# Performance work log

Hardware: AMD Instinct MI355X
Metric: run time of the kernel (lower is better)

Reference implementation:

```python
import jax, jax.numpy as jnp
import numpy as np

HID, NH, HD, KTS = 512, 8, 64, 4
BATCH, SEQ = 2, 1024
CLIP, AMIN, AMAX = 2.0, 1e-4, 0.9995
ROPE_BASE = 10000.0


def _rmsnorm(x, w, eps=1e-5):
    rms = jnp.sqrt(jnp.mean(x * x, axis=-1, keepdims=True) + eps)
    return x / rms * w


def _rope(q, k, base=ROPE_BASE):
    # q,k: [B,T,H,D], D even -> rotate-half formulation (split halves, not interleaved)
    T, D = q.shape[1], q.shape[-1]
    half = D // 2
    pos = jnp.arange(T, dtype=q.dtype)
    inv_freq = 1.0 / (base ** (jnp.arange(half, dtype=q.dtype) / half))
    ang = pos[:, None] * inv_freq[None, :]            # [T, half]
    cos = jnp.cos(ang)[None, :, None, :]
    sin = jnp.sin(ang)[None, :, None, :]
    def rot(x):
        x1, x2 = x[..., :half], x[..., half:]
        return jnp.concatenate([x1 * cos - x2 * sin, x1 * sin + x2 * cos], axis=-1)
    return rot(q), rot(k)


def setup_inputs() -> dict:
    key = jax.random.key(0)
    ks = jax.random.split(key, 10)
    def xavier(k, shape):
        lim = float(np.sqrt(6.0 / (shape[0] + shape[1])))
        return jax.random.uniform(k, shape, jnp.float32, -lim, lim)
    x = jax.random.normal(ks[0], (BATCH, SEQ, HID), jnp.float32)
    mask = jnp.ones((BATCH, SEQ), jnp.int32)
    qW = xavier(ks[1], (HID, HID))
    kW = xavier(ks[2], (HID, HID))
    vW = xavier(ks[3], (HID, HID))
    oW = xavier(ks[4], (HID, HID))
    ob = jnp.zeros((HID,), jnp.float32)
    # alpha bias from geometric half-lives [32,128,512,2048]
    half_lives = np.array([32.0 * (4.0 ** i) for i in range(KTS)], dtype=np.float64)
    alphas = np.clip(np.exp(-np.log(2.0) / half_lives), AMIN, AMAX)
    alphas = np.tile(alphas, NH)
    ab = jnp.asarray(np.log(alphas / (1.0 - alphas)), jnp.float32)
    aW = 0.01 * jax.random.normal(ks[5], (NH * KTS, HID), jnp.float32)
    mW = 0.01 * jax.random.normal(ks[6], (NH * KTS, HID), jnp.float32)
    mb = jnp.zeros((NH * KTS,), jnp.float32)
    in_w = jnp.ones((HID,), jnp.float32)
    kn_w = jnp.ones((HD,), jnp.float32)
    vn_w = jnp.ones((HD,), jnp.float32)
    ln_w = jnp.ones((HID,), jnp.float32)
    ln_b = jnp.zeros((HID,), jnp.float32)
    return dict(x=x, in_w=in_w, qW=qW, kW=kW, vW=vW, aW=aW, ab=ab, mW=mW, mb=mb,
                oW=oW, ob=ob, kn_w=kn_w, vn_w=vn_w, ln_w=ln_w, ln_b=ln_b, mask=mask)


def reference(x, in_w, qW, kW, vW, aW, ab, mW, mb, oW, ob, kn_w, vn_w, ln_w, ln_b, mask):
    B, T, _ = x.shape
    xn = _rmsnorm(x, in_w)
    q = (xn @ qW.T).reshape(B, T, NH, HD)
    k = (xn @ kW.T).reshape(B, T, NH, HD)
    v = (xn @ vW.T).reshape(B, T, NH, HD)
    q, k = _rope(q, k)
    k = _rmsnorm(k, kn_w)
    v = _rmsnorm(v, vn_w)
    alpha = jnp.clip(jax.nn.sigmoid(xn @ aW.T + ab), AMIN, AMAX).reshape(B, T, NH, KTS)
    mix = jax.nn.softmax((xn @ mW.T + mb).reshape(B, T, NH, KTS), axis=-1)
    m = mask.astype(jnp.float32)
    c = float(np.sqrt(HD)) * CLIP

    def step(h, inp):
        # h: [B,H,K,D,D] fp32 state; delta-rule write + multi-timescale decay + norm clip
        q_t, k_t, v_t, a_t, mx_t, m_t = inp
        outer = (k_t * m_t[:, None, None])[:, :, None, :, None] * v_t[:, :, None, None, :]
        h = h * a_t[..., None, None] + outer
        norm = jnp.sqrt(jnp.sum(h * h, axis=(-2, -1), keepdims=True))
        h = h * jnp.minimum(c / (norm + 1e-6), 1.0)
        y = jnp.einsum('bhd,bhkde->bhke', q_t, h)
        return h, jnp.einsum('bhk,bhkd->bhd', mx_t, y)

    h0 = jnp.zeros((B, NH, KTS, HD, HD), jnp.float32)
    tm = lambda a: jnp.moveaxis(a, 1, 0)  # time-major
    xs = (tm(q), tm(k), tm(v), tm(alpha), tm(mix), m.T)
    _, ys = jax.lax.scan(jax.checkpoint(step), h0, xs)  # ys: [T,B,H,D]
    y = jnp.moveaxis(ys, 0, 1).reshape(B, T, HID)
    out = y @ oW.T + ob  # dropout p=0 (eval)
    r = x + out
    mu = jnp.mean(r, axis=-1, keepdims=True)
    var = jnp.mean((r - mu) ** 2, axis=-1, keepdims=True)
    return (r - mu) / jnp.sqrt(var + 1e-5) * ln_w + ln_b
```

## Files before the change

### kernel.cpp

```cpp
#include <hip/hip_runtime.h>
#include <math.h>

#define SEQT 1024
#define NTOK 2048
#define HIDN 512
#define NHD 8
#define HDIM 64
#define KTSN 4

__device__ __forceinline__ float wred(float v) {
#pragma unroll
  for (int off = 32; off; off >>= 1) v += __shfl_xor(v, off, 64);
  return v;
}

template <int CTRL>
__device__ __forceinline__ float rra(float v) {
  return v + __int_as_float(__builtin_amdgcn_update_dpp(
                 0, __float_as_int(v), CTRL, 0xf, 0xf, true));
}
__device__ __forceinline__ float rlane(float v, int l) {
  return __int_as_float(__builtin_amdgcn_readlane(__float_as_int(v), l));
}
__device__ __forceinline__ float wsum64_fast(float v) {
  v = rra<0x121>(v);
  v = rra<0x122>(v);
  v = rra<0x124>(v);
  v = rra<0x128>(v);
  return (rlane(v, 0) + rlane(v, 16)) + (rlane(v, 32) + rlane(v, 48));
}

__global__ __launch_bounds__(256) void k_rmsnorm_in(
    const float* __restrict__ x, const float* __restrict__ w, float* __restrict__ xn) {
  int m = blockIdx.x;
  int tid = threadIdx.x;
  const float* row = x + (size_t)m * HIDN;
  float2 v = *(const float2*)(row + tid * 2);
  float ss = wred(v.x * v.x + v.y * v.y);
  __shared__ float red[4];
  int lane = tid & 63, wv = tid >> 6;
  if (lane == 0) red[wv] = ss;
  __syncthreads();
  float tot = red[0] + red[1] + red[2] + red[3];
  float inv = rsqrtf(tot * (1.0f / HIDN) + 1e-5f);
  float2 wv2 = *(const float2*)(w + tid * 2);
  float2 o;
  o.x = v.x * inv * wv2.x;
  o.y = v.y * inv * wv2.y;
  *(float2*)(xn + (size_t)m * HIDN + tid * 2) = o;
}

__global__ __launch_bounds__(256) void k_gemm_nt(
    const float* __restrict__ A, const float* __restrict__ B, float* __restrict__ C, int N) {
  __shared__ __align__(16) float As[32][68];
  __shared__ __align__(16) float Bs[32][68];
  int tid = threadIdx.x;
  int m0 = blockIdx.x * 64, n0 = blockIdx.y * 64;
  int tm = tid >> 4, tn = tid & 15;
  float acc[4][4] = {};
  int rr = tid >> 2, cc = (tid & 3) * 8;
  for (int k0 = 0; k0 < HIDN; k0 += 32) {
    const float* s0 = A + (size_t)(m0 + rr) * HIDN + k0 + cc;
    float4 a0 = *(const float4*)s0;
    float4 a1 = *(const float4*)(s0 + 4);
    As[cc + 0][rr] = a0.x; As[cc + 1][rr] = a0.y; As[cc + 2][rr] = a0.z; As[cc + 3][rr] = a0.w;
    As[cc + 4][rr] = a1.x; As[cc + 5][rr] = a1.y; As[cc + 6][rr] = a1.z; As[cc + 7][rr] = a1.w;
    int bn = n0 + rr;
    float4 b0 = make_float4(0.f, 0.f, 0.f, 0.f), b1 = make_float4(0.f, 0.f, 0.f, 0.f);
    if (bn < N) {
      const float* s1 = B + (size_t)bn * HIDN + k0 + cc;
      b0 = *(const float4*)s1;
      b1 = *(const float4*)(s1 + 4);
    }
    Bs[cc + 0][rr] = b0.x; Bs[cc + 1][rr] = b0.y; Bs[cc + 2][rr] = b0.z; Bs[cc + 3][rr] = b0.w;
    Bs[cc + 4][rr] = b1.x; Bs[cc + 5][rr] = b1.y; Bs[cc + 6][rr] = b1.z; Bs[cc + 7][rr] = b1.w;
    __syncthreads();
#pragma unroll
    for (int kk = 0; kk < 32; ++kk) {
      float4 a4 = *(const float4*)&As[kk][tm * 4];
      float4 b4 = *(const float4*)&Bs[kk][tn * 4];
      float aa[4] = {a4.x, a4.y, a4.z, a4.w};
      float bb[4] = {b4.x, b4.y, b4.z, b4.w};
#pragma unroll
      for (int i = 0; i < 4; ++i)
#pragma unroll
        for (int j = 0; j < 4; ++j) acc[i][j] += aa[i] * bb[j];
    }
    __syncthreads();
  }
#pragma unroll
  for (int i = 0; i < 4; ++i) {
    int mr = m0 + tm * 4 + i;
#pragma unroll
    for (int j = 0; j < 4; ++j) {
      int nc = n0 + tn * 4 + j;
      if (nc < N) C[(size_t)mr * N + nc] = acc[i][j];
    }
  }
}

__global__ __launch_bounds__(256) void k_rope_table(float2* __restrict__ tab) {
  int idx = blockIdx.x * 256 + threadIdx.x;
  int t = idx >> 5, j = idx & 31;
  float invf = (float)exp2(-(double)j * (13.287712379549449 / 32.0));
  float ang = (float)t * invf;
  double s, c;
  sincos((double)ang, &s, &c);
  tab[idx] = make_float2((float)c, (float)s);
}

__global__ __launch_bounds__(256) void k_postproc(
    const float* __restrict__ q_in, const float* __restrict__ k_in, const float* __restrict__ v_in,
    const float* __restrict__ a_pre, const float* __restrict__ m_pre,
    const float* __restrict__ ab, const float* __restrict__ mb,
    const float* __restrict__ kn_w, const float* __restrict__ vn_w,
    const float2* __restrict__ tab,
    float* __restrict__ qh, float* __restrict__ kh, float* __restrict__ vh,
    float* __restrict__ av, float* __restrict__ mv) {
  int wid = blockIdx.x * 4 + (threadIdx.x >> 6);
  int lane = threadIdx.x & 63;
  int b = wid >> 13;
  int rem = wid & 8191;
  int t = rem >> 3;
  int h = rem & 7;
  size_t src = (size_t)(b * SEQT + t) * HIDN + h * HDIM + lane;
  float qv = q_in[src], kv = k_in[src], vv = v_in[src];
  float2 cs = tab[t * 32 + (lane & 31)];
  float qpart = __shfl_xor(qv, 32, 64);
  float kpart = __shfl_xor(kv, 32, 64);
  float qr = (lane < 32) ? (qv * cs.x - qpart * cs.y) : (qpart * cs.y + qv * cs.x);
  float kr = (lane < 32) ? (kv * cs.x - kpart * cs.y) : (kpart * cs.y + kv * cs.x);
  float kss = wred(kr * kr);
  float kn = kr * rsqrtf(kss * (1.0f / HDIM) + 1e-5f) * kn_w[lane];
  float vss = wred(vv * vv);
  float vn = vv * rsqrtf(vss * (1.0f / HDIM) + 1e-5f) * vn_w[lane];
  size_t dst = ((size_t)(b * NHD + h) * SEQT + t) * HDIM + lane;
  qh[dst] = qr;
  kh[dst] = kn;
  vh[dst] = vn;
  if (lane < 4) {
    int col = h * 4 + lane;
    float pa = a_pre[(size_t)(b * SEQT + t) * 32 + col] + ab[col];
    float al = 1.0f / (1.0f + expf(-pa));
    al = fminf(fmaxf(al, 1e-4f), 0.9995f);
    float pm = m_pre[(size_t)(b * SEQT + t) * 32 + col] + mb[col];
    float mx = pm;
    mx = fmaxf(mx, __shfl_xor(mx, 1, 64));
    mx = fmaxf(mx, __shfl_xor(mx, 2, 64));
    float e = expf(pm - mx);
    float sum = e;
    sum += __shfl_xor(sum, 1, 64);
    sum += __shfl_xor(sum, 2, 64);
    size_t adst = ((size_t)(b * NHD + h) * KTSN + lane) * SEQT + t;
    av[adst] = al;
    mv[adst] = e / sum;
  }
}

#define G16(X) \
  X(0, 0) X(1, 1) X(2, 2) X(3, 3) X(4, 0) X(5, 1) X(6, 2) X(7, 3) \
  X(8, 0) X(9, 1) X(10, 2) X(11, 3) X(12, 0) X(13, 1) X(14, 2) X(15, 3)

#define DECLH(g, a) float h##g = 0.f;

#define UPDH(g, a)                                \
  {                                               \
    float ks = rlane(kqC, g);                     \
    h##g = fmaf(h##g, ag, ks * vem);              \
    sq##a = fmaf(h##g, h##g, sq##a);              \
  }

#define YUPH(g, a)                                \
  {                                               \
    float qs = rlane(kqC, 16 + (g));              \
    y##a = fmaf(qs, h##g, y##a);                  \
  }

__global__ __launch_bounds__(256, 1) void k_scan(
    const float* __restrict__ qh, const float* __restrict__ kh, const float* __restrict__ vh,
    const float* __restrict__ av, const float* __restrict__ mv, const int* __restrict__ mask,
    float* __restrict__ y0p, float* __restrict__ y1p, float* __restrict__ y2p,
    float* __restrict__ y3p) {
  int c = blockIdx.x;
  int kt = c & 3;
  int bh = c >> 2;
  int b = bh >> 3;
  int h = bh & 7;
  int tid = threadIdx.x;
  int w = tid >> 6;
  int lane = tid & 63;
  int dbase = w * 16;

  const float* kp = kh + (size_t)bh * SEQT * HDIM;
  const float* qp = qh + (size_t)bh * SEQT * HDIM;
  const float* vp = vh + (size_t)bh * SEQT * HDIM;
  const float* ap = av + (size_t)c * SEQT;
  const float* mp = mv + (size_t)c * SEQT;
  const int* mk = mask + (size_t)b * SEQT;
  float* ysel = (kt == 0) ? y0p : (kt == 1) ? y1p : (kt == 2) ? y2p : y3p;
  float* ypo = ysel + (size_t)(b * SEQT) * HIDN + h * HDIM + lane;

  __shared__ __align__(16) float sqb[2][4];
  __shared__ __align__(16) float ypart[2][4][64];

  G16(DECLH)
  float gprev = 1.0f;

  int off = lane & 15;
  const float* kqbase = ((lane >> 4) & 1) ? qp : kp;
  int kqidx = dbase + off;

  float kqC = kqbase[kqidx];
  float kqD = kqbase[(size_t)1 * HDIM + kqidx];
  float kqE = kqbase[(size_t)2 * HDIM + kqidx];
  float vC = vp[lane];
  float vD = vp[(size_t)1 * HDIM + lane];
  float vE = vp[(size_t)2 * HDIM + lane];
  float aC = ap[0], aD = ap[1], aE = ap[2];
  float mxC = mp[0], mxD = mp[1], mxE = mp[2];
  float mC = (float)mk[0], mD = (float)mk[1], mE = (float)mk[2];

  for (int t = 0; t < SEQT; ++t) {
    int t3 = t + 3;
    if (t3 > SEQT - 1) t3 = SEQT - 1;
    float kqN = kqbase[(size_t)t3 * HDIM + kqidx];
    float vN = vp[(size_t)t3 * HDIM + lane];
    float aN = ap[t3];
    float mxN = mp[t3];
    float mN = (float)mk[t3];

    float ag = aC * gprev;
    float vem = vC * mC;
    float sq0 = 0.f, sq1 = 0.f, sq2 = 0.f, sq3 = 0.f;
    G16(UPDH)
    float y0 = 0.f, y1 = 0.f, y2 = 0.f, y3 = 0.f;
    G16(YUPH)
    float sqw = wsum64_fast((sq0 + sq1) + (sq2 + sq3));
    float yp = (y0 + y1) + (y2 + y3);

    int P = t & 1;
    if (lane == 0) sqb[P][w] = sqw;
    ypart[P][w][lane] = yp;
    __syncthreads();
    float4 sq4 = *(const float4*)&sqb[P][0];
    float sqt = (sq4.x + sq4.y) + (sq4.z + sq4.w);
    float g = fminf(16.0f * rsqrtf(sqt), 1.0f);
    if (w == 0) {
      float ys = (ypart[P][0][lane] + ypart[P][1][lane]) +
                 (ypart[P][2][lane] + ypart[P][3][lane]);
      ypo[(size_t)t * HIDN] = (mxC * g) * ys;
    }
    gprev = g;

    kqC = kqD; kqD = kqE; kqE = kqN;
    vC = vD; vD = vE; vE = vN;
    aC = aD; aD = aE; aE = aN;
    mxC = mxD; mxD = mxE; mxE = mxN;
    mC = mD; mD = mE; mE = mN;
  }
}

__global__ __launch_bounds__(256) void k_gemm_out(
    const float* __restrict__ y0, const float* __restrict__ y1,
    const float* __restrict__ y2, const float* __restrict__ y3,
    const float* __restrict__ oW, const float* __restrict__ ob,
    const float* __restrict__ x, float* __restrict__ r) {
  __shared__ __align__(16) float As[32][68];
  __shared__ __align__(16) float Bs[32][68];
  int tid = threadIdx.x;
  int m0 = blockIdx.x * 64, n0 = blockIdx.y * 64;
  int tm = tid >> 4, tn = tid & 15;
  float acc[4][4] = {};
  int rr = tid >> 2, cc = (tid & 3) * 8;
  for (int k0 = 0; k0 < HIDN; k0 += 32) {
    size_t aoff = (size_t)(m0 + rr) * HIDN + k0 + cc;
#pragma unroll
    for (int half = 0; half < 2; ++half) {
      size_t sh = aoff + half * 4;
      float4 p0 = *(const float4*)(y0 + sh);
      float4 p1 = *(const float4*)(y1 + sh);
      float4 p2 = *(const float4*)(y2 + sh);
      float4 p3 = *(const float4*)(y3 + sh);
      int cbase = cc + half * 4;
      As[cbase + 0][rr] = p0.x + p1.x + p2.x + p3.x;
      As[cbase + 1][rr] = p0.y + p1.y + p2.y + p3.y;
      As[cbase + 2][rr] = p0.z + p1.z + p2.z + p3.z;
      As[cbase + 3][rr] = p0.w + p1.w + p2.w + p3.w;
    }
    const float* s1 = oW + (size_t)(n0 + rr) * HIDN + k0 + cc;
    float4 b0 = *(const float4*)s1;
    float4 b1 = *(const float4*)(s1 + 4);
    Bs[cc + 0][rr] = b0.x; Bs[cc + 1][rr] = b0.y; Bs[cc + 2][rr] = b0.z; Bs[cc + 3][rr] = b0.w;
    Bs[cc + 4][rr] = b1.x; Bs[cc + 5][rr] = b1.y; Bs[cc + 6][rr] = b1.z; Bs[cc + 7][rr] = b1.w;
    __syncthreads();
#pragma unroll
    for (int kk = 0; kk < 32; ++kk) {
      float4 a4 = *(const float4*)&As[kk][tm * 4];
      float4 b4 = *(const float4*)&Bs[kk][tn * 4];
      float aa[4] = {a4.x, a4.y, a4.z, a4.w};
      float bb[4] = {b4.x, b4.y, b4.z, b4.w};
#pragma unroll
      for (int i = 0; i < 4; ++i)
#pragma unroll
        for (int j = 0; j < 4; ++j) acc[i][j] += aa[i] * bb[j];
    }
    __syncthreads();
  }
#pragma unroll
  for (int i = 0; i < 4; ++i) {
    int mr = m0 + tm * 4 + i;
#pragma unroll
    for (int j = 0; j < 4; ++j) {
      int nc = n0 + tn * 4 + j;
      r[(size_t)mr * HIDN + nc] = x[(size_t)mr * HIDN + nc] + acc[i][j] + ob[nc];
    }
  }
}

__global__ __launch_bounds__(256) void k_layernorm(
    const float* __restrict__ r, const float* __restrict__ w, const float* __restrict__ bb,
    float* __restrict__ out) {
  int m = blockIdx.x;
  int tid = threadIdx.x;
  const float* row = r + (size_t)m * HIDN;
  float2 v = *(const float2*)(row + tid * 2);
  float s = wred(v.x + v.y);
  float ss = wred(v.x * v.x + v.y * v.y);
  __shared__ float r1[4], r2[4];
  int lane = tid & 63, wv = tid >> 6;
  if (lane == 0) {
    r1[wv] = s;
    r2[wv] = ss;
  }
  __syncthreads();
  float S = r1[0] + r1[1] + r1[2] + r1[3];
  float SS = r2[0] + r2[1] + r2[2] + r2[3];
  float mu = S * (1.0f / HIDN);
  float var = SS * (1.0f / HIDN) - mu * mu;
  float inv = rsqrtf(var + 1e-5f);
  float2 w2 = *(const float2*)(w + tid * 2);
  float2 b2 = *(const float2*)(bb + tid * 2);
  float2 o;
  o.x = (v.x - mu) * inv * w2.x + b2.x;
  o.y = (v.y - mu) * inv * w2.y + b2.y;
  *(float2*)(out + (size_t)m * HIDN + tid * 2) = o;
}

extern "C" void kernel_launch(void* const* d_in, const int* in_sizes, int n_in,
                              void* d_out, int out_size, void* d_ws, size_t ws_size,
                              hipStream_t stream) {
  const float* x = (const float*)d_in[0];
  const float* in_w = (const float*)d_in[1];
  const float* qW = (const float*)d_in[2];
  const float* kW = (const float*)d_in[3];
  const float* vW = (const float*)d_in[4];
  const float* aW = (const float*)d_in[5];
  const float* ab = (const float*)d_in[6];
  const float* mW = (const float*)d_in[7];
  const float* mb = (const float*)d_in[8];
  const float* oW = (const float*)d_in[9];
  const float* ob = (const float*)d_in[10];
  const float* kn_w = (const float*)d_in[11];
  const float* vn_w = (const float*)d_in[12];
  const float* ln_w = (const float*)d_in[13];
  const float* ln_b = (const float*)d_in[14];
  const int* mask = (const int*)d_in[15];

  float* ws = (float*)d_ws;
  float* xn = ws + 0;
  float* qb = ws + 1048576;
  float* kb = ws + 2097152;
  float* vb = ws + 3145728;
  float* apre = ws + 4194304;
  float* mpre = ws + 4259840;
  float2* tab = (float2*)(ws + 4325376);
  float* qh = ws + 4390912;
  float* kh = ws + 5439488;
  float* vh = ws + 6488064;
  float* avv = ws + 7536640;
  float* mvv = ws + 7602176;
  float* y3 = ws + 7667712;
  float* y0 = qb;
  float* y1 = kb;
  float* y2 = vb;
  float* rr = xn;

  k_rmsnorm_in<<<NTOK, 256, 0, stream>>>(x, in_w, xn);
  k_rope_table<<<128, 256, 0, stream>>>(tab);
  dim3 gBig(32, 8);
  k_gemm_nt<<<gBig, 256, 0, stream>>>(xn, qW, qb, 512);
  k_gemm_nt<<<gBig, 256, 0, stream>>>(xn, kW, kb, 512);
  k_gemm_nt<<<gBig, 256, 0, stream>>>(xn, vW, vb, 512);
  dim3 gSmall(32, 1);
  k_gemm_nt<<<gSmall, 256, 0, stream>>>(xn, aW, apre, 32);
  k_gemm_nt<<<gSmall, 256, 0, stream>>>(xn, mW, mpre, 32);
  k_postproc<<<4096, 256, 0, stream>>>(qb, kb, vb, apre, mpre, ab, mb, kn_w, vn_w, tab,
                                       qh, kh, vh, avv, mvv);
  k_scan<<<64, 256, 0, stream>>>(qh, kh, vh, avv, mvv, mask, y0, y1, y2, y3);
  k_gemm_out<<<gBig, 256, 0, stream>>>(y0, y1, y2, y3, oW, ob, x, rr);
  k_layernorm<<<NTOK, 256, 0, stream>>>(rr, ln_w, ln_b, (float*)d_out);
  (void)in_sizes; (void)n_in; (void)out_size; (void)ws_size;
}
```

Measured before the change: 792.3 us.

## Merge four timescale scans into one block per batch-head

The scan kernel now runs one block per (batch, head) that carries all four timescale states, instead of one block per (batch, head, timescale). The k/q/v loads, lane broadcasts and the per-step barrier are shared across the four states, and each wave writes the output for one timescale. This raises per-thread work and register use and cuts the grid from 64 to 16 blocks, so most CUs sit idle. Each block's serial step does four times the arithmetic in exchange for fewer redundant loads and fewer barriers overall.

After: 1.215 ms. 53.3% more time.

```diff
diff --git a/kernel.cpp b/kernel.cpp
--- a/kernel.cpp
+++ b/kernel.cpp
@@ -157,23 +157,34 @@
   }
 }
 
-#define G16(X) \
-  X(0, 0) X(1, 1) X(2, 2) X(3, 3) X(4, 0) X(5, 1) X(6, 2) X(7, 3) \
-  X(8, 0) X(9, 1) X(10, 2) X(11, 3) X(12, 0) X(13, 1) X(14, 2) X(15, 3)
-
-#define DECLH(g, a) float h##g = 0.f;
-
-#define UPDH(g, a)                                \
+#define G16P(X) \
+  X(0, 0) X(1, 1) X(2, 0) X(3, 1) X(4, 0) X(5, 1) X(6, 0) X(7, 1) \
+  X(8, 0) X(9, 1) X(10, 0) X(11, 1) X(12, 0) X(13, 1) X(14, 0) X(15, 1)
+
+#define DECLH(g, p) \
+  float hA##g = 0.f, hB##g = 0.f, hC##g = 0.f, hD##g = 0.f;
+
+#define UPD(g, p)                                 \
   {                                               \
-    float ks = rlane(kqC, g);                     \
-    h##g = fmaf(h##g, ag, ks * vem);              \
-    sq##a = fmaf(h##g, h##g, sq##a);              \
-  }
-
-#define YUPH(g, a)                                \
+    float ks = rlane(kqs0, g);                    \
+    float kv = ks * vem;                          \
+    hA##g = fmaf(hA##g, agA, kv);                 \
+    sqA##p = fmaf(hA##g, hA##g, sqA##p);          \
+    hB##g = fmaf(hB##g, agB, kv);                 \
+    sqB##p = fmaf(hB##g, hB##g, sqB##p);          \
+    hC##g = fmaf(hC##g, agC, kv);                 \
+    sqC##p = fmaf(hC##g, hC##g, sqC##p);          \
+    hD##g = fmaf(hD##g, agD, kv);                 \
+    sqD##p = fmaf(hD##g, hD##g, sqD##p);          \
+  }
+
+#define YUP(g, p)                                 \
   {                                               \
-    float qs = rlane(kqC, 16 + (g));              \
-    y##a = fmaf(qs, h##g, y##a);                  \
+    float qs = rlane(kqs0, 16 + (g));             \
+    yA##p = fmaf(qs, hA##g, yA##p);               \
+    yB##p = fmaf(qs, hB##g, yB##p);               \
+    yC##p = fmaf(qs, hC##g, yC##p);               \
+    yD##p = fmaf(qs, hD##g, yD##p);               \
   }
 
 __global__ __launch_bounds__(256, 1) void k_scan(
@@ -181,9 +192,7 @@
     const float* __restrict__ av, const float* __restrict__ mv, const int* __restrict__ mask,
     float* __restrict__ y0p, float* __restrict__ y1p, float* __restrict__ y2p,
     float* __restrict__ y3p) {
-  int c = blockIdx.x;
-  int kt = c & 3;
-  int bh = c >> 2;
+  int bh = blockIdx.x;
   int b = bh >> 3;
   int h = bh & 7;
   int tid = threadIdx.x;
@@ -194,69 +203,93 @@
   const float* kp = kh + (size_t)bh * SEQT * HDIM;
   const float* qp = qh + (size_t)bh * SEQT * HDIM;
   const float* vp = vh + (size_t)bh * SEQT * HDIM;
-  const float* ap = av + (size_t)c * SEQT;
-  const float* mp = mv + (size_t)c * SEQT;
+  const float* apA = av + (size_t)(bh * 4 + 0) * SEQT;
+  const float* apB = av + (size_t)(bh * 4 + 1) * SEQT;
+  const float* apC = av + (size_t)(bh * 4 + 2) * SEQT;
+  const float* apD = av + (size_t)(bh * 4 + 3) * SEQT;
+  const float* mpA = mv + (size_t)(bh * 4 + 0) * SEQT;
+  const float* mpB = mv + (size_t)(bh * 4 + 1) * SEQT;
+  const float* mpC = mv + (size_t)(bh * 4 + 2) * SEQT;
+  const float* mpD = mv + (size_t)(bh * 4 + 3) * SEQT;
   const int* mk = mask + (size_t)b * SEQT;
-  float* ysel = (kt == 0) ? y0p : (kt == 1) ? y1p : (kt == 2) ? y2p : y3p;
-  float* ypo = ysel + (size_t)(b * SEQT) * HIDN + h * HDIM + lane;
-
-  __shared__ __align__(16) float sqb[2][4];
-  __shared__ __align__(16) float ypart[2][4][64];
-
-  G16(DECLH)
-  float gprev = 1.0f;
+  float* ywsel = (w == 0) ? y0p : (w == 1) ? y1p : (w == 2) ? y2p : y3p;
+  float* ypoW = ywsel + (size_t)(b * SEQT) * HIDN + h * HDIM + lane;
+
+  __shared__ __align__(16) float4 sqb[2][4];
+  __shared__ __align__(16) float ypart[2][4][4][64];
+
+  G16P(DECLH)
+  float gA = 1.f, gB = 1.f, gC = 1.f, gD = 1.f;
 
   int off = lane & 15;
   const float* kqbase = ((lane >> 4) & 1) ? qp : kp;
   int kqidx = dbase + off;
 
-  float kqC = kqbase[kqidx];
-  float kqD = kqbase[(size_t)1 * HDIM + kqidx];
-  float kqE = kqbase[(size_t)2 * HDIM + kqidx];
-  float vC = vp[lane];
-  float vD = vp[(size_t)1 * HDIM + lane];
-  float vE = vp[(size_t)2 * HDIM + lane];
-  float aC = ap[0], aD = ap[1], aE = ap[2];
-  float mxC = mp[0], mxD = mp[1], mxE = mp[2];
-  float mC = (float)mk[0], mD = (float)mk[1], mE = (float)mk[2];
+  float kqs0 = kqbase[kqidx];
+  float kqs1 = kqbase[(size_t)1 * HDIM + kqidx];
+  float kqs2 = kqbase[(size_t)2 * HDIM + kqidx];
+  float vs0 = vp[lane], vs1 = vp[HDIM + lane], vs2 = vp[2 * HDIM + lane];
+  float ms0 = (float)mk[0], ms1 = (float)mk[1], ms2 = (float)mk[2];
+  float aAs0 = apA[0], aAs1 = apA[1], aAs2 = apA[2];
+  float aBs0 = apB[0], aBs1 = apB[1], aBs2 = apB[2];
+  float aCs0 = apC[0], aCs1 = apC[1], aCs2 = apC[2];
+  float aDs0 = apD[0], aDs1 = apD[1], aDs2 = apD[2];
+  float mxAs0 = mpA[0], mxAs1 = mpA[1], mxAs2 = mpA[2];
+  float mxBs0 = mpB[0], mxBs1 = mpB[1], mxBs2 = mpB[2];
+  float mxCs0 = mpC[0], mxCs1 = mpC[1], mxCs2 = mpC[2];
+  float mxDs0 = mpD[0], mxDs1 = mpD[1], mxDs2 = mpD[2];
 
   for (int t = 0; t < SEQT; ++t) {
     int t3 = t + 3;
     if (t3 > SEQT - 1) t3 = SEQT - 1;
     float kqN = kqbase[(size_t)t3 * HDIM + kqidx];
     float vN = vp[(size_t)t3 * HDIM + lane];
-    float aN = ap[t3];
-    float mxN = mp[t3];
     float mN = (float)mk[t3];
-
-    float ag = aC * gprev;
-    float vem = vC * mC;
-    float sq0 = 0.f, sq1 = 0.f, sq2 = 0.f, sq3 = 0.f;
-    G16(UPDH)
-    float y0 = 0.f, y1 = 0.f, y2 = 0.f, y3 = 0.f;
-    G16(YUPH)
-    float sqw = wsum64_fast((sq0 + sq1) + (sq2 + sq3));
-    float yp = (y0 + y1) + (y2 + y3);
+    float aAN = apA[t3], aBN = apB[t3], aCN = apC[t3], aDN = apD[t3];
+    float mxAN = mpA[t3], mxBN = mpB[t3], mxCN = mpC[t3], mxDN = mpD[t3];
+
+    float vem = vs0 * ms0;
+    float agA = aAs0 * gA, agB = aBs0 * gB, agC = aCs0 * gC, agD = aDs0 * gD;
+    float sqA0 = 0.f, sqA1 = 0.f, sqB0 = 0.f, sqB1 = 0.f;
+    float sqC0 = 0.f, sqC1 = 0.f, sqD0 = 0.f, sqD1 = 0.f;
+    G16P(UPD)
+    float yA0 = 0.f, yA1 = 0.f, yB0 = 0.f, yB1 = 0.f;
+    float yC0 = 0.f, yC1 = 0.f, yD0 = 0.f, yD1 = 0.f;
+    G16P(YUP)
+    float wsA = wsum64_fast(sqA0 + sqA1);
+    float wsB = wsum64_fast(sqB0 + sqB1);
+    float wsC = wsum64_fast(sqC0 + sqC1);
+    float wsD = wsum64_fast(sqD0 + sqD1);
 
     int P = t & 1;
-    if (lane == 0) sqb[P][w] = sqw;
-    ypart[P][w][lane] = yp;
+    if (lane == 0) sqb[P][w] = make_float4(wsA, wsB, wsC, wsD);
+    ypart[P][0][w][lane] = yA0 + yA1;
+    ypart[P][1][w][lane] = yB0 + yB1;
+    ypart[P][2][w][lane] = yC0 + yC1;
+    ypart[P][3][w][lane] = yD0 + yD1;
     __syncthreads();
-    float4 sq4 = *(const float4*)&sqb[P][0];
-    float sqt = (sq4.x + sq4.y) + (sq4.z + sq4.w);
-    float g = fminf(16.0f * rsqrtf(sqt), 1.0f);
-    if (w == 0) {
-      float ys = (ypart[P][0][lane] + ypart[P][1][lane]) +
-                 (ypart[P][2][lane] + ypart[P][3][lane]);
-      ypo[(size_t)t * HIDN] = (mxC * g) * ys;
-    }
-    gprev = g;
-
-    kqC = kqD; kqD = kqE; kqE = kqN;
-    vC = vD; vD = vE; vE = vN;
-    aC = aD; aD = aE; aE = aN;
-    mxC = mxD; mxD = mxE; mxE = mxN;
-    mC = mD; mD = mE; mE = mN;
+    float4 s0 = sqb[P][0], s1 = sqb[P][1], s2 = sqb[P][2], s3 = sqb[P][3];
+    gA = fminf(16.0f * rsqrtf((s0.x + s1.x) + (s2.x + s3.x)), 1.0f);
+    gB = fminf(16.0f * rsqrtf((s0.y + s1.y) + (s2.y + s3.y)), 1.0f);
+    gC = fminf(16.0f * rsqrtf((s0.z + s1.z) + (s2.z + s3.z)), 1.0f);
+    gD = fminf(16.0f * rsqrtf((s0.w + s1.w) + (s2.w + s3.w)), 1.0f);
+    float ys = (ypart[P][w][0][lane] + ypart[P][w][1][lane]) +
+               (ypart[P][w][2][lane] + ypart[P][w][3][lane]);
+    float mxsel = (w == 0) ? mxAs0 : (w == 1) ? mxBs0 : (w == 2) ? mxCs0 : mxDs0;
+    float gsel = (w == 0) ? gA : (w == 1) ? gB : (w == 2) ? gC : gD;
+    ypoW[(size_t)t * HIDN] = (mxsel * gsel) * ys;
+
+    kqs0 = kqs1; kqs1 = kqs2; kqs2 = kqN;
+    vs0 = vs1; vs1 = vs2; vs2 = vN;
+    ms0 = ms1; ms1 = ms2; ms2 = mN;
+    aAs0 = aAs1; aAs1 = aAs2; aAs2 = aAN;
+    aBs0 = aBs1; aBs1 = aBs2; aBs2 = aBN;
+    aCs0 = aCs1; aCs1 = aCs2; aCs2 = aCN;
+    aDs0 = aDs1; aDs1 = aDs2; aDs2 = aDN;
+    mxAs0 = mxAs1; mxAs1 = mxAs2; mxAs2 = mxAN;
+    mxBs0 = mxBs1; mxBs1 = mxBs2; mxBs2 = mxBN;
+    mxCs0 = mxCs1; mxCs1 = mxCs2; mxCs2 = mxCN;
+    mxDs0 = mxDs1; mxDs1 = mxDs2; mxDs2 = mxDN;
   }
 }
 
@@ -396,7 +429,7 @@
   k_gemm_nt<<<gSmall, 256, 0, stream>>>(xn, mW, mpre, 32);
   k_postproc<<<4096, 256, 0, stream>>>(qb, kb, vb, apre, mpre, ab, mb, kn_w, vn_w, tab,
                                        qh, kh, vh, avv, mvv);
-  k_scan<<<64, 256, 0, stream>>>(qh, kh, vh, avv, mvv, mask, y0, y1, y2, y3);
+  k_scan<<<16, 256, 0, stream>>>(qh, kh, vh, avv, mvv, mask, y0, y1, y2, y3);
   k_gemm_out<<<gBig, 256, 0, stream>>>(y0, y1, y2, y3, oW, ob, x, rr);
   k_layernorm<<<NTOK, 256, 0, stream>>>(rr, ln_w, ln_b, (float*)d_out);
   (void)in_sizes; (void)n_in; (void)out_size; (void)ws_size;
```

## Compute scan norm and output incrementally to shorten the per-step critical path

Applied to the files above, without the earlier changes.

The recurrence is rewritten algebraically so the per-step state norm is tracked as a^2·||H||^2 + 2a·k^T H v + ||k||^2||v||^2. The output uses a·q^T H + (q·k)·v. The needed projections k_{t+1}^T H and q_{t+1}^T H are computed right after each state update and reduced across waves for the next step. Postproc now precomputes per-token q·k and ||k||^2||v||^2. The aim is to take the full squared-norm reduction and its barrier off the dependency chain between the update and the clip. This adds extra matvec work per step and may drift numerically, since the norm is accumulated incrementally rather than recomputed.

Result: slower. 927.5 us (+17.1%).

```diff
diff --git a/kernel.cpp b/kernel.cpp
--- a/kernel.cpp
+++ b/kernel.cpp
@@ -28,6 +28,10 @@
   v = rra<0x124>(v);
   v = rra<0x128>(v);
   return (rlane(v, 0) + rlane(v, 16)) + (rlane(v, 32) + rlane(v, 48));
+}
+
+__device__ __forceinline__ void lds_barrier() {
+  asm volatile("s_waitcnt lgkmcnt(0)\n\ts_barrier" ::: "memory");
 }
 
 __global__ __launch_bounds__(256) void k_rmsnorm_in(
@@ -116,7 +120,8 @@
     const float* __restrict__ kn_w, const float* __restrict__ vn_w,
     const float2* __restrict__ tab,
     float* __restrict__ qh, float* __restrict__ kh, float* __restrict__ vh,
-    float* __restrict__ av, float* __restrict__ mv) {
+    float* __restrict__ av, float* __restrict__ mv,
+    float* __restrict__ qkd, float* __restrict__ kvq) {
   int wid = blockIdx.x * 4 + (threadIdx.x >> 6);
   int lane = threadIdx.x & 63;
   int b = wid >> 13;
@@ -138,6 +143,14 @@
   qh[dst] = qr;
   kh[dst] = kn;
   vh[dst] = vn;
+  float knss = wred(kn * kn);
+  float vnss = wred(vn * vn);
+  float qkdot = wred(qr * kn);
+  if (lane == 0) {
+    size_t sdst = (size_t)(b * NHD + h) * SEQT + t;
+    qkd[sdst] = qkdot;
+    kvq[sdst] = knss * vnss;
+  }
   if (lane < 4) {
     int col = h * 4 + lane;
     float pa = a_pre[(size_t)(b * SEQT + t) * 32 + col] + ab[col];
@@ -157,28 +170,29 @@
   }
 }
 
-#define G16(X) \
+#define G16P(X) \
   X(0, 0) X(1, 1) X(2, 2) X(3, 3) X(4, 0) X(5, 1) X(6, 2) X(7, 3) \
   X(8, 0) X(9, 1) X(10, 2) X(11, 3) X(12, 0) X(13, 1) X(14, 2) X(15, 3)
 
 #define DECLH(g, a) float h##g = 0.f;
-
-#define UPDH(g, a)                                \
+#define DECLKK(g, a) float kk##g;
+#define SEEDKK(g, a) kk##g = rlane(kqs0, (g));
+
+#define HUP(g, a) h##g = fmaf(h##g, ag, kk##g * vem);
+
+#define MV(g, a)                                  \
   {                                               \
-    float ks = rlane(kqC, g);                     \
-    h##g = fmaf(h##g, ag, ks * vem);              \
-    sq##a = fmaf(h##g, h##g, sq##a);              \
-  }
-
-#define YUPH(g, a)                                \
-  {                                               \
-    float qs = rlane(kqC, 16 + (g));              \
-    y##a = fmaf(qs, h##g, y##a);                  \
+    float kn_ = rlane(kqs1, (g));                 \
+    float qn_ = rlane(kqs1, 16 + (g));            \
+    kh##a = fmaf(kn_, h##g, kh##a);               \
+    pa##a = fmaf(qn_, h##g, pa##a);               \
+    kk##g = kn_;                                  \
   }
 
 __global__ __launch_bounds__(256, 1) void k_scan(
     const float* __restrict__ qh, const float* __restrict__ kh, const float* __restrict__ vh,
     const float* __restrict__ av, const float* __restrict__ mv, const int* __restrict__ mask,
+    const float* __restrict__ qkd, const float* __restrict__ kvq,
     float* __restrict__ y0p, float* __restrict__ y1p, float* __restrict__ y2p,
     float* __restrict__ y3p) {
   int c = blockIdx.x;
@@ -196,31 +210,42 @@
   const float* vp = vh + (size_t)bh * SEQT * HDIM;
   const float* ap = av + (size_t)c * SEQT;
   const float* mp = mv + (size_t)c * SEQT;
+  const float* qkp = qkd + (size_t)bh * SEQT;
+  const float* kvp = kvq + (size_t)bh * SEQT;
   const int* mk = mask + (size_t)b * SEQT;
   float* ysel = (kt == 0) ? y0p : (kt == 1) ? y1p : (kt == 2) ? y2p : y3p;
   float* ypo = ysel + (size_t)(b * SEQT) * HIDN + h * HDIM + lane;
 
-  __shared__ __align__(16) float sqb[2][4];
-  __shared__ __align__(16) float ypart[2][4][64];
-
-  G16(DECLH)
+  __shared__ __align__(16) float zb[2][4];
+  __shared__ __align__(16) float pex[2][4][64];
+
+  G16P(DECLH)
+  G16P(DECLKK)
   float gprev = 1.0f;
+  float usq = 0.0f;
 
   int off = lane & 15;
   const float* kqbase = ((lane >> 4) & 1) ? qp : kp;
   int kqidx = dbase + off;
 
-  float kqC = kqbase[kqidx];
-  float kqD = kqbase[(size_t)1 * HDIM + kqidx];
-  float kqE = kqbase[(size_t)2 * HDIM + kqidx];
-  float vC = vp[lane];
-  float vD = vp[(size_t)1 * HDIM + lane];
-  float vE = vp[(size_t)2 * HDIM + lane];
-  float aC = ap[0], aD = ap[1], aE = ap[2];
-  float mxC = mp[0], mxD = mp[1], mxE = mp[2];
-  float mC = (float)mk[0], mD = (float)mk[1], mE = (float)mk[2];
+  float kqs0 = kqbase[kqidx];
+  float kqs1 = kqbase[(size_t)1 * HDIM + kqidx];
+  float kqs2 = kqbase[(size_t)2 * HDIM + kqidx];
+  float vs0 = vp[lane], vs1 = vp[HDIM + lane], vs2 = vp[2 * HDIM + lane];
+  float a0 = ap[0], a1 = ap[1], a2 = ap[2];
+  float mx0 = mp[0], mx1 = mp[1], mx2 = mp[2];
+  float m0 = (float)mk[0], m1 = (float)mk[1], m2 = (float)mk[2];
+  float qk0 = qkp[0], qk1 = qkp[1], qk2 = qkp[2];
+  float kv0 = kvp[0], kv1 = kvp[1], kv2 = kvp[2];
+
+  G16P(SEEDKK)
+
+  if (lane == 0) zb[0][w] = 0.f;
+  pex[0][w][lane] = 0.f;
+  lds_barrier();
 
   for (int t = 0; t < SEQT; ++t) {
+    int P = t & 1;
     int t3 = t + 3;
     if (t3 > SEQT - 1) t3 = SEQT - 1;
     float kqN = kqbase[(size_t)t3 * HDIM + kqidx];
@@ -228,35 +253,45 @@
     float aN = ap[t3];
     float mxN = mp[t3];
     float mN = (float)mk[t3];
-
-    float ag = aC * gprev;
-    float vem = vC * mC;
-    float sq0 = 0.f, sq1 = 0.f, sq2 = 0.f, sq3 = 0.f;
-    G16(UPDH)
-    float y0 = 0.f, y1 = 0.f, y2 = 0.f, y3 = 0.f;
-    G16(YUPH)
-    float sqw = wsum64_fast((sq0 + sq1) + (sq2 + sq3));
-    float yp = (y0 + y1) + (y2 + y3);
-
-    int P = t & 1;
-    if (lane == 0) sqb[P][w] = sqw;
-    ypart[P][w][lane] = yp;
-    __syncthreads();
-    float4 sq4 = *(const float4*)&sqb[P][0];
-    float sqt = (sq4.x + sq4.y) + (sq4.z + sq4.w);
-    float g = fminf(16.0f * rsqrtf(sqt), 1.0f);
+    float qkN = qkp[t3];
+    float kvN = kvp[t3];
+
+    float ag = a0 * gprev;
+    float vem = vs0 * m0;
+    G16P(HUP)
+
+    float4 z4 = *(const float4*)&zb[P][0];
+    float zt = (z4.x + z4.y) + (z4.z + z4.w);
+    float usqn = fmaf(ag * ag, usq, fmaf(2.0f * ag * m0, zt, (m0 * m0) * kv0));
+    usqn = fmaxf(usqn, 0.0f);
+    float g = fminf(16.0f * rsqrtf(usqn), 1.0f);
+
+    float kh0 = 0.f, kh1 = 0.f, kh2 = 0.f, kh3 = 0.f;
+    float pa0 = 0.f, pa1 = 0.f, pa2 = 0.f, pa3 = 0.f;
+    G16P(MV)
+    float khs = (kh0 + kh1) + (kh2 + kh3);
+    float pp = (pa0 + pa1) + (pa2 + pa3);
+    float zp = wsum64_fast(khs * vs1);
+
     if (w == 0) {
-      float ys = (ypart[P][0][lane] + ypart[P][1][lane]) +
-                 (ypart[P][2][lane] + ypart[P][3][lane]);
-      ypo[(size_t)t * HIDN] = (mxC * g) * ys;
-    }
+      float ps = (pex[P][0][lane] + pex[P][1][lane]) +
+                 (pex[P][2][lane] + pex[P][3][lane]);
+      ypo[(size_t)t * HIDN] = (g * mx0) * fmaf(ag, ps, (m0 * qk0) * vs0);
+    }
+
+    if (lane == 0) zb[P ^ 1][w] = zp;
+    pex[P ^ 1][w][lane] = pp;
+    lds_barrier();
+
     gprev = g;
-
-    kqC = kqD; kqD = kqE; kqE = kqN;
-    vC = vD; vD = vE; vE = vN;
-    aC = aD; aD = aE; aE = aN;
-    mxC = mxD; mxD = mxE; mxE = mxN;
-    mC = mD; mD = mE; mE = mN;
+    usq = usqn;
+    kqs0 = kqs1; kqs1 = kqs2; kqs2 = kqN;
+    vs0 = vs1; vs1 = vs2; vs2 = vN;
+    a0 = a1; a1 = a2; a2 = aN;
+    mx0 = mx1; mx1 = mx2; mx2 = mxN;
+    m0 = m1; m1 = m2; m2 = mN;
+    qk0 = qk1; qk1 = qk2; qk2 = qkN;
+    kv0 = kv1; kv1 = kv2; kv2 = kvN;
   }
 }
 
@@ -384,6 +419,8 @@
   float* y1 = kb;
   float* y2 = vb;
   float* rr = xn;
+  float* qkd = ws + 0;
+  float* kvq = ws + 16384;
 
   k_rmsnorm_in<<<NTOK, 256, 0, stream>>>(x, in_w, xn);
   k_rope_table<<<128, 256, 0, stream>>>(tab);
@@ -395,8 +432,8 @@
   k_gemm_nt<<<gSmall, 256, 0, stream>>>(xn, aW, apre, 32);
   k_gemm_nt<<<gSmall, 256, 0, stream>>>(xn, mW, mpre, 32);
   k_postproc<<<4096, 256, 0, stream>>>(qb, kb, vb, apre, mpre, ab, mb, kn_w, vn_w, tab,
-                                       qh, kh, vh, avv, mvv);
-  k_scan<<<64, 256, 0, stream>>>(qh, kh, vh, avv, mvv, mask, y0, y1, y2, y3);
+                                       qh, kh, vh, avv, mvv, qkd, kvq);
+  k_scan<<<64, 256, 0, stream>>>(qh, kh, vh, avv, mvv, mask, qkd, kvq, y0, y1, y2, y3);
   k_gemm_out<<<gBig, 256, 0, stream>>>(y0, y1, y2, y3, oW, ob, x, rr);
   k_layernorm<<<NTOK, 256, 0, stream>>>(rr, ln_w, ln_b, (float*)d_out);
   (void)in_sizes; (void)n_in; (void)out_size; (void)ws_size;
```
